# Kernel optimization log

Hardware: AMD Instinct MI355X
Metric: run time of the kernel (lower is better)

The kernel has to match this reference:

```python
import jax, jax.numpy as jnp
import numpy as np

N_NODES = 100000


def gcn_conv(x, W, b, src, dst, n):
    # PyG GCNConv: add self-loops, symmetric deg^-1/2 normalization,
    # transform then gather/scatter-add aggregate.
    loop = jnp.arange(n, dtype=src.dtype)
    s = jnp.concatenate([src, loop])
    d = jnp.concatenate([dst, loop])
    deg = jax.ops.segment_sum(jnp.ones_like(d, dtype=x.dtype), d, num_segments=n)
    dinv = jnp.where(deg > 0, 1.0 / jnp.sqrt(deg), 0.0)
    norm = dinv[s] * dinv[d]                      # [E+N]
    h = x @ W                                     # [N, out]
    msgs = h[s] * norm[:, None]                   # gather + scale
    out = jax.ops.segment_sum(msgs, d, num_segments=n)  # scatter-add
    return out + b


def setup_inputs() -> dict:
    key = jax.random.key(0)
    k1, k2, k3, k4 = jax.random.split(key, 4)
    F_in, H, D = 128, 16, 128
    x = jax.random.normal(k1, (N_NODES, F_in), dtype=jnp.float32)
    edge_index = jax.random.randint(k2, (2, 1600000), 0, N_NODES, dtype=jnp.int64)
    W1 = jax.random.normal(k3, (F_in, H), dtype=jnp.float32) / np.sqrt(F_in)
    b1 = jnp.zeros((H,), dtype=jnp.float32)
    W2 = jax.random.normal(k4, (H, D), dtype=jnp.float32) / np.sqrt(H)
    b2 = jnp.zeros((D,), dtype=jnp.float32)
    return {"x": x, "edge_index": edge_index, "W1": W1, "b1": b1, "W2": W2, "b2": b2}


def reference(x, edge_index, W1, b1, W2, b2):
    src, dst = edge_index[0], edge_index[1]
    n = x.shape[0]
    h = jax.nn.relu(gcn_conv(x, W1, b1, src, dst, n))
    out = jax.nn.relu(gcn_conv(h, W2, b2, src, dst, n))
    return out
```

## Files before the change

kernel.cpp:

```cpp
#include <hip/hip_runtime.h>
#include <hip/hip_fp16.h>
#include <stdint.h>

#define F_IN  128
#define HID   16
#define F_OUT 128
#define NBK   512
#define NBLK  512
#define BCAP  4096
#define CHUNK_MAX 4096
#define EPT   16

__device__ __forceinline__ int bucket_of(int d, int N) {
    return (int)(((long long)d * NBK) / N);
}
__device__ __forceinline__ int bucket_lo(int b, int N) {
    return (int)(((long long)b * N + NBK - 1) / NBK);
}

__global__ void __launch_bounds__(256) k_partf(
        const int* __restrict__ ei, int* __restrict__ bcur,
        uint32_t* __restrict__ pairs, int E, int N) {
    __shared__ int lh[NBK];
    __shared__ int lofs[NBK];
    __shared__ int lcur[NBK];
    __shared__ int gbase[NBK];
    __shared__ int lnlo[NBK];
    __shared__ int loff[256];
    __shared__ uint32_t spairs[CHUNK_MAX];
    __shared__ uint16_t sbkt[CHUNK_MAX];

    int blk = blockIdx.x, t = threadIdx.x;
    int C = (E + NBLK - 1) / NBLK;
    int e0 = blk * C;
    int e1 = e0 + C; if (e1 > E) e1 = E;
    int ecnt = e1 - e0;

    for (int i = t; i < NBK; i += 256) { lh[i] = 0; lnlo[i] = bucket_lo(i, N); }
    __syncthreads();

    int es[EPT], ed[EPT], eb[EPT];
#pragma unroll
    for (int k = 0; k < EPT; ++k) {
        int e = e0 + k * 256 + t;
        if (e < e1) {
            es[k] = ei[e];
            ed[k] = ei[E + e];
            eb[k] = bucket_of(ed[k], N);
            atomicAdd(&lh[eb[k]], 1);
        } else eb[k] = -1;
    }
    __syncthreads();

    int a0 = lh[2 * t], a1 = lh[2 * t + 1];
    int s2 = a0 + a1;
    loff[t] = s2;
    __syncthreads();
    for (int o = 1; o < 256; o <<= 1) {
        int a = (t >= o) ? loff[t - o] : 0;
        __syncthreads();
        loff[t] += a;
        __syncthreads();
    }
    int excl = loff[t] - s2;
    lofs[2 * t]     = excl;
    lofs[2 * t + 1] = excl + a0;
    lcur[2 * t]     = excl;
    lcur[2 * t + 1] = excl + a0;
    __syncthreads();

    for (int w = 0; w < NBK; w += 256) {
        int i = (t + w + blk) & (NBK - 1);
        int h = lh[i];
        gbase[i] = h ? atomicAdd(&bcur[i], h) : 0;
    }

#pragma unroll
    for (int k = 0; k < EPT; ++k) {
        if (eb[k] >= 0) {
            int b = eb[k];
            int idx = atomicAdd(&lcur[b], 1);
            spairs[idx] = ((uint32_t)es[k] << 10) | (uint32_t)(ed[k] - lnlo[b]);
            sbkt[idx]   = (uint16_t)b;
        }
    }
    __syncthreads();

    for (int i = t; i < ecnt; i += 256) {
        int b = sbkt[i];
        int pos = gbase[b] + (i - lofs[b]);
        if (pos < BCAP)
            pairs[(size_t)b * BCAP + pos] = spairs[i];
    }
}

__global__ void __launch_bounds__(256) k_csr2(
        const uint32_t* __restrict__ pairs, const int* __restrict__ bcur,
        int* __restrict__ row_start, int* __restrict__ cnt,
        float* __restrict__ dinv, int* __restrict__ srcs, int N) {
    __shared__ int lcnt[256];
    __shared__ int loff[256];
    __shared__ int lcur[256];
    int b = blockIdx.x, t = threadIdx.x;
    int base = b * BCAP;
    int ec = bcur[b]; if (ec > BCAP) ec = BCAP;
    int nlo = bucket_lo(b, N);
    int nhi = bucket_lo(b + 1, N); if (nhi > N) nhi = N;
    int nn = nhi - nlo;
    lcnt[t] = 0;
    __syncthreads();
    for (int e = t; e < ec; e += 256)
        atomicAdd(&lcnt[pairs[base + e] & 1023u], 1);
    __syncthreads();
    int v = lcnt[t];
    int pv = (v + 3) & ~3;
    loff[t] = pv;
    __syncthreads();
    for (int o = 1; o < 256; o <<= 1) {
        int a = (t >= o) ? loff[t - o] : 0;
        __syncthreads();
        loff[t] += a;
        __syncthreads();
    }
    if (t < nn) {
        int gs = base + (loff[t] - pv);
        row_start[nlo + t] = gs;
        cnt[nlo + t]       = v;
        dinv[nlo + t]      = rsqrtf((float)(v + 1));
        lcur[t]            = gs;
    }
    __syncthreads();
    for (int e = t; e < ec; e += 256) {
        uint32_t p = pairs[base + e];
        int pos = atomicAdd(&lcur[p & 1023u], 1);
        srcs[pos] = (int)(p >> 10);
    }
}

#define XP1 132
__global__ void __launch_bounds__(256) k_transform1(
        const float* __restrict__ x, const float* __restrict__ W1,
        const float* __restrict__ dinv, __half* __restrict__ g1, int n) {
    __shared__ float sX[32 * XP1];
    __shared__ float sWt[HID * XP1];
    int t = threadIdx.x;
    int node0 = blockIdx.x * 32;
    for (int i = t; i < F_IN * HID; i += 256) {
        int k = i >> 4, f = i & 15;
        sWt[f * XP1 + k] = W1[i];
    }
    const float4* x4 = (const float4*)(x + (size_t)node0 * F_IN);
    int nrem = n - node0;
#pragma unroll
    for (int j = 0; j < 4; ++j) {
        int idx4 = t + j * 256;
        int nl = idx4 >> 5;
        int kk = (idx4 & 31) * 4;
        float4 v = make_float4(0.f, 0.f, 0.f, 0.f);
        if (nl < nrem) v = x4[idx4];
        *(float4*)&sX[nl * XP1 + kk] = v;
    }
    __syncthreads();
    int f  = t & 7;
    int nl = t >> 3;
    float a0 = 0.f, a1 = 0.f;
    const float* xr  = &sX[nl * XP1];
    const float* wr0 = &sWt[f * XP1];
    const float* wr1 = &sWt[(f + 8) * XP1];
#pragma unroll 4
    for (int k = 0; k < F_IN; k += 4) {
        float4 xv = *(const float4*)(xr + k);
        float4 w0 = *(const float4*)(wr0 + k);
        float4 w1 = *(const float4*)(wr1 + k);
        a0 += xv.x * w0.x + xv.y * w0.y + xv.z * w0.z + xv.w * w0.w;
        a1 += xv.x * w1.x + xv.y * w1.y + xv.z * w1.z + xv.w * w1.w;
    }
    int node = node0 + nl;
    if (node < n) {
        float di = dinv[node];
        g1[(size_t)node * HID + f]     = __float2half(di * a0);
        g1[(size_t)node * HID + f + 8] = __float2half(di * a1);
    }
}

__device__ __forceinline__ void add_h8(float* __restrict__ acc, const __half* __restrict__ ptr) {
    uint4 u = *(const uint4*)ptr;
    const __half2* h = (const __half2*)&u;
#pragma unroll
    for (int q = 0; q < 4; ++q) {
        float2 f = __half22float2(h[q]);
        acc[2 * q]     += f.x;
        acc[2 * q + 1] += f.y;
    }
}

template<bool EP1>
__global__ void __launch_bounds__(256) k_gather_h(
        const __half* __restrict__ g, const int* __restrict__ srcs,
        const int* __restrict__ row_start, const int* __restrict__ cnt,
        const float* __restrict__ dinv, const float* __restrict__ b1,
        __half* __restrict__ outb, int n) {
    int t = blockIdx.x * blockDim.x + threadIdx.x;
    int node = t >> 1;
    int p = t & 1;
    if (node >= n) return;
    int rs  = row_start[node];
    int deg = cnt[node];
    float acc[8];
    {
        uint4 u = *(const uint4*)(g + (size_t)node * HID + p * 8);
        const __half2* h = (const __half2*)&u;
#pragma unroll
        for (int q = 0; q < 4; ++q) {
            float2 f = __half22float2(h[q]);
            acc[2 * q] = f.x; acc[2 * q + 1] = f.y;
        }
    }
    int j = 0;
    for (; j + 8 <= deg; j += 8) {
        int4 ia = *(const int4*)(srcs + rs + j);
        int4 ib = *(const int4*)(srcs + rs + j + 4);
        add_h8(acc, g + (size_t)ia.x * HID + p * 8);
        add_h8(acc, g + (size_t)ia.y * HID + p * 8);
        add_h8(acc, g + (size_t)ia.z * HID + p * 8);
        add_h8(acc, g + (size_t)ia.w * HID + p * 8);
        add_h8(acc, g + (size_t)ib.x * HID + p * 8);
        add_h8(acc, g + (size_t)ib.y * HID + p * 8);
        add_h8(acc, g + (size_t)ib.z * HID + p * 8);
        add_h8(acc, g + (size_t)ib.w * HID + p * 8);
    }
    if (j + 4 <= deg) {
        int4 ia = *(const int4*)(srcs + rs + j);
        add_h8(acc, g + (size_t)ia.x * HID + p * 8);
        add_h8(acc, g + (size_t)ia.y * HID + p * 8);
        add_h8(acc, g + (size_t)ia.z * HID + p * 8);
        add_h8(acc, g + (size_t)ia.w * HID + p * 8);
        j += 4;
    }
    for (; j < deg; ++j)
        add_h8(acc, g + (size_t)srcs[rs + j] * HID + p * 8);
    if (EP1) {
        float di = dinv[node];
#pragma unroll
        for (int i = 0; i < 8; ++i)
            acc[i] = di * fmaxf(di * acc[i] + b1[p * 8 + i], 0.0f);
    }
    uint4 o;
    __half2* oh = (__half2*)&o;
#pragma unroll
    for (int q = 0; q < 4; ++q)
        oh[q] = __floats2half2_rn(acc[2 * q], acc[2 * q + 1]);
    *(uint4*)(outb + (size_t)node * HID + p * 8) = o;
}

__global__ void __launch_bounds__(256) k_transform2(
        const __half* __restrict__ agg, const float* __restrict__ W2,
        const float* __restrict__ b2, const float* __restrict__ dinv,
        float* __restrict__ out, int n) {
    int t = threadIdx.x;
    int d = t & 127;
    int h = t >> 7;
    int node0 = blockIdx.x * 32;
    float wcol[HID];
#pragma unroll
    for (int f = 0; f < HID; ++f) wcol[f] = W2[f * F_OUT + d];
    float bd = b2[d];
#pragma unroll 4
    for (int i = 0; i < 16; ++i) {
        int node = node0 + h + 2 * i;
        if (node >= n) continue;
        const uint4* av = (const uint4*)(agg + (size_t)node * HID);
        uint4 u0 = av[0], u1 = av[1];
        const __half2* h0 = (const __half2*)&u0;
        const __half2* h1 = (const __half2*)&u1;
        float s = 0.f;
#pragma unroll
        for (int q = 0; q < 4; ++q) {
            float2 f0 = __half22float2(h0[q]);
            float2 f1 = __half22float2(h1[q]);
            s += f0.x * wcol[2 * q]     + f0.y * wcol[2 * q + 1];
            s += f1.x * wcol[8 + 2 * q] + f1.y * wcol[9 + 2 * q];
        }
        out[(size_t)node * F_OUT + d] = fmaxf(dinv[node] * s + bd, 0.0f);
    }
}

extern "C" void kernel_launch(void* const* d_in, const int* in_sizes, int n_in,
                              void* d_out, int out_size, void* d_ws, size_t ws_size,
                              hipStream_t stream) {
    const float* x  = (const float*)d_in[0];
    const int*   ei = (const int*)d_in[1];
    const float* W1 = (const float*)d_in[2];
    const float* b1 = (const float*)d_in[3];
    const float* W2 = (const float*)d_in[4];
    const float* b2 = (const float*)d_in[5];
    float* out = (float*)d_out;

    const int N = in_sizes[0] / F_IN;
    const int E = in_sizes[1] / 2;

    float* dinv      = (float*)d_ws;
    int*   cnt       = (int*)(dinv + N);
    int*   row_start = cnt + N;
    int*   bcur      = row_start + N;
    int*   srcs      = bcur + NBK;
    uintptr_t xb = (uintptr_t)(srcs + (size_t)NBK * BCAP + 64);
    xb = (xb + 15) & ~(uintptr_t)15;
    uint32_t* pairs = (uint32_t*)xb;
    __half* bufA = (__half*)xb;
    __half* bufB = bufA + (size_t)N * HID;

    hipMemsetAsync(bcur, 0, NBK * sizeof(int), stream);
    k_partf<<<NBLK, 256, 0, stream>>>(ei, bcur, pairs, E, N);
    k_csr2 <<<NBK, 256, 0, stream>>>(pairs, bcur, row_start, cnt, dinv, srcs, N);

    k_transform1<<<(N + 31) / 32, 256, 0, stream>>>(x, W1, dinv, bufA, N);
    k_gather_h<true> <<<((size_t)N * 2 + 255) / 256, 256, 0, stream>>>(
        bufA, srcs, row_start, cnt, dinv, b1, bufB, N);
    k_gather_h<false><<<((size_t)N * 2 + 255) / 256, 256, 0, stream>>>(
        bufB, srcs, row_start, cnt, dinv, b1, bufA, N);
    k_transform2<<<(N + 31) / 32, 256, 0, stream>>>(bufA, W2, b2, dinv, out, N);
}
```

Before: 211.0 us.

## Fuse all GCN phases into one cooperative persistent kernel with grid syncs

Replaces the memset and six separate kernel launches with a single cooperative kernel of 512 blocks. The phases (partition, CSR build, transform1, two gathers, transform2) run back to back, separated by grid.sync, and use grid-stride loops. This removes launch overhead and inter-kernel gaps. In exchange it caps parallelism at 512 blocks for the gather and transform phases, and it pays grid-barrier costs. If the cooperative launch fails, it falls back to the multi-kernel path.

```diff
diff --git a/kernel.cpp b/kernel.cpp
--- a/kernel.cpp
+++ b/kernel.cpp
@@ -1,6 +1,9 @@
 #include <hip/hip_runtime.h>
 #include <hip/hip_fp16.h>
+#include <hip/hip_cooperative_groups.h>
 #include <stdint.h>
+
+namespace cg = cooperative_groups;
 
 #define F_IN  128
 #define HID   16
@@ -10,6 +13,9 @@
 #define BCAP  4096
 #define CHUNK_MAX 4096
 #define EPT   16
+#define XP1   132
+
+static_assert(NBLK == NBK, "csr phase needs block==bucket");
 
 __device__ __forceinline__ int bucket_of(int d, int N) {
     return (int)(((long long)d * NBK) / N);
@@ -18,25 +24,28 @@
     return (int)(((long long)b * N + NBK - 1) / NBK);
 }
 
-__global__ void __launch_bounds__(256) k_partf(
-        const int* __restrict__ ei, int* __restrict__ bcur,
-        uint32_t* __restrict__ pairs, int E, int N) {
-    __shared__ int lh[NBK];
-    __shared__ int lofs[NBK];
-    __shared__ int lcur[NBK];
-    __shared__ int gbase[NBK];
-    __shared__ int lnlo[NBK];
-    __shared__ int loff[256];
-    __shared__ uint32_t spairs[CHUNK_MAX];
-    __shared__ uint16_t sbkt[CHUNK_MAX];
-
-    int blk = blockIdx.x, t = threadIdx.x;
+struct SmemPartf {
+    int lh[NBK], lofs[NBK], lcur[NBK], gbase[NBK], lnlo[NBK];
+    int loff[256];
+    uint32_t spairs[CHUNK_MAX];
+    uint16_t sbkt[CHUNK_MAX];
+};
+struct SmemCsr { int lcnt[256], loff[256], lcur[256]; };
+struct SmemT1  { float sX[32 * XP1]; float sWt[HID * XP1]; };
+
+constexpr unsigned SMEM_BYTES =
+    sizeof(SmemPartf) > sizeof(SmemT1) ? sizeof(SmemPartf) : sizeof(SmemT1);
+
+__device__ void phase_partf(char* smem, int blk, int t,
+                            const int* __restrict__ ei, int* __restrict__ bcur,
+                            uint32_t* __restrict__ pairs, int E, int N) {
+    SmemPartf* sp = (SmemPartf*)smem;
     int C = (E + NBLK - 1) / NBLK;
     int e0 = blk * C;
     int e1 = e0 + C; if (e1 > E) e1 = E;
     int ecnt = e1 - e0;
 
-    for (int i = t; i < NBK; i += 256) { lh[i] = 0; lnlo[i] = bucket_lo(i, N); }
+    for (int i = t; i < NBK; i += 256) { sp->lh[i] = 0; sp->lnlo[i] = bucket_lo(i, N); }
     __syncthreads();
 
     int es[EPT], ed[EPT], eb[EPT];
@@ -47,139 +56,137 @@
             es[k] = ei[e];
             ed[k] = ei[E + e];
             eb[k] = bucket_of(ed[k], N);
-            atomicAdd(&lh[eb[k]], 1);
+            atomicAdd(&sp->lh[eb[k]], 1);
         } else eb[k] = -1;
     }
     __syncthreads();
 
-    int a0 = lh[2 * t], a1 = lh[2 * t + 1];
+    int a0 = sp->lh[2 * t], a1 = sp->lh[2 * t + 1];
     int s2 = a0 + a1;
-    loff[t] = s2;
+    sp->loff[t] = s2;
     __syncthreads();
     for (int o = 1; o < 256; o <<= 1) {
-        int a = (t >= o) ? loff[t - o] : 0;
-        __syncthreads();
-        loff[t] += a;
-        __syncthreads();
-    }
-    int excl = loff[t] - s2;
-    lofs[2 * t]     = excl;
-    lofs[2 * t + 1] = excl + a0;
-    lcur[2 * t]     = excl;
-    lcur[2 * t + 1] = excl + a0;
+        int a = (t >= o) ? sp->loff[t - o] : 0;
+        __syncthreads();
+        sp->loff[t] += a;
+        __syncthreads();
+    }
+    int excl = sp->loff[t] - s2;
+    sp->lofs[2 * t]     = excl;
+    sp->lofs[2 * t + 1] = excl + a0;
+    sp->lcur[2 * t]     = excl;
+    sp->lcur[2 * t + 1] = excl + a0;
     __syncthreads();
 
     for (int w = 0; w < NBK; w += 256) {
         int i = (t + w + blk) & (NBK - 1);
-        int h = lh[i];
-        gbase[i] = h ? atomicAdd(&bcur[i], h) : 0;
+        int h = sp->lh[i];
+        sp->gbase[i] = h ? atomicAdd(&bcur[i], h) : 0;
     }
 
 #pragma unroll
     for (int k = 0; k < EPT; ++k) {
         if (eb[k] >= 0) {
             int b = eb[k];
-            int idx = atomicAdd(&lcur[b], 1);
-            spairs[idx] = ((uint32_t)es[k] << 10) | (uint32_t)(ed[k] - lnlo[b]);
-            sbkt[idx]   = (uint16_t)b;
+            int idx = atomicAdd(&sp->lcur[b], 1);
+            sp->spairs[idx] = ((uint32_t)es[k] << 10) | (uint32_t)(ed[k] - sp->lnlo[b]);
+            sp->sbkt[idx]   = (uint16_t)b;
         }
     }
     __syncthreads();
 
     for (int i = t; i < ecnt; i += 256) {
-        int b = sbkt[i];
-        int pos = gbase[b] + (i - lofs[b]);
+        int b = sp->sbkt[i];
+        int pos = sp->gbase[b] + (i - sp->lofs[b]);
         if (pos < BCAP)
-            pairs[(size_t)b * BCAP + pos] = spairs[i];
-    }
-}
-
-__global__ void __launch_bounds__(256) k_csr2(
-        const uint32_t* __restrict__ pairs, const int* __restrict__ bcur,
-        int* __restrict__ row_start, int* __restrict__ cnt,
-        float* __restrict__ dinv, int* __restrict__ srcs, int N) {
-    __shared__ int lcnt[256];
-    __shared__ int loff[256];
-    __shared__ int lcur[256];
-    int b = blockIdx.x, t = threadIdx.x;
+            pairs[(size_t)b * BCAP + pos] = sp->spairs[i];
+    }
+}
+
+__device__ void phase_csr(char* smem, int b, int t,
+                          const uint32_t* __restrict__ pairs, const int* __restrict__ bcur,
+                          int* __restrict__ row_start, int* __restrict__ cnt,
+                          float* __restrict__ dinv, int* __restrict__ srcs, int N) {
+    SmemCsr* sc = (SmemCsr*)smem;
     int base = b * BCAP;
     int ec = bcur[b]; if (ec > BCAP) ec = BCAP;
     int nlo = bucket_lo(b, N);
     int nhi = bucket_lo(b + 1, N); if (nhi > N) nhi = N;
     int nn = nhi - nlo;
-    lcnt[t] = 0;
+    sc->lcnt[t] = 0;
     __syncthreads();
     for (int e = t; e < ec; e += 256)
-        atomicAdd(&lcnt[pairs[base + e] & 1023u], 1);
-    __syncthreads();
-    int v = lcnt[t];
+        atomicAdd(&sc->lcnt[pairs[base + e] & 1023u], 1);
+    __syncthreads();
+    int v = sc->lcnt[t];
     int pv = (v + 3) & ~3;
-    loff[t] = pv;
+    sc->loff[t] = pv;
     __syncthreads();
     for (int o = 1; o < 256; o <<= 1) {
-        int a = (t >= o) ? loff[t - o] : 0;
-        __syncthreads();
-        loff[t] += a;
+        int a = (t >= o) ? sc->loff[t - o] : 0;
+        __syncthreads();
+        sc->loff[t] += a;
         __syncthreads();
     }
     if (t < nn) {
-        int gs = base + (loff[t] - pv);
+        int gs = base + (sc->loff[t] - pv);
         row_start[nlo + t] = gs;
         cnt[nlo + t]       = v;
         dinv[nlo + t]      = rsqrtf((float)(v + 1));
-        lcur[t]            = gs;
+        sc->lcur[t]        = gs;
     }
     __syncthreads();
     for (int e = t; e < ec; e += 256) {
         uint32_t p = pairs[base + e];
-        int pos = atomicAdd(&lcur[p & 1023u], 1);
+        int pos = atomicAdd(&sc->lcur[p & 1023u], 1);
         srcs[pos] = (int)(p >> 10);
     }
 }
 
-#define XP1 132
-__global__ void __launch_bounds__(256) k_transform1(
-        const float* __restrict__ x, const float* __restrict__ W1,
-        const float* __restrict__ dinv, __half* __restrict__ g1, int n) {
-    __shared__ float sX[32 * XP1];
-    __shared__ float sWt[HID * XP1];
-    int t = threadIdx.x;
-    int node0 = blockIdx.x * 32;
+__device__ void phase_t1(char* smem, int blk, int nblk, int t,
+                         const float* __restrict__ x, const float* __restrict__ W1,
+                         const float* __restrict__ dinv, __half* __restrict__ g1, int n) {
+    SmemT1* st = (SmemT1*)smem;
     for (int i = t; i < F_IN * HID; i += 256) {
         int k = i >> 4, f = i & 15;
-        sWt[f * XP1 + k] = W1[i];
-    }
-    const float4* x4 = (const float4*)(x + (size_t)node0 * F_IN);
-    int nrem = n - node0;
-#pragma unroll
-    for (int j = 0; j < 4; ++j) {
-        int idx4 = t + j * 256;
-        int nl = idx4 >> 5;
-        int kk = (idx4 & 31) * 4;
-        float4 v = make_float4(0.f, 0.f, 0.f, 0.f);
-        if (nl < nrem) v = x4[idx4];
-        *(float4*)&sX[nl * XP1 + kk] = v;
-    }
-    __syncthreads();
+        st->sWt[f * XP1 + k] = W1[i];
+    }
+    int nvb = (n + 31) / 32;
     int f  = t & 7;
     int nl = t >> 3;
-    float a0 = 0.f, a1 = 0.f;
-    const float* xr  = &sX[nl * XP1];
-    const float* wr0 = &sWt[f * XP1];
-    const float* wr1 = &sWt[(f + 8) * XP1];
+    for (int vb = blk; vb < nvb; vb += nblk) {
+        __syncthreads();
+        int node0 = vb * 32;
+        const float4* x4 = (const float4*)(x + (size_t)node0 * F_IN);
+        int nrem = n - node0;
+#pragma unroll
+        for (int j = 0; j < 4; ++j) {
+            int idx4 = t + j * 256;
+            int nl2 = idx4 >> 5;
+            int kk = (idx4 & 31) * 4;
+            float4 v = make_float4(0.f, 0.f, 0.f, 0.f);
+            if (nl2 < nrem) v = x4[idx4];
+            *(float4*)&st->sX[nl2 * XP1 + kk] = v;
+        }
+        __syncthreads();
+        float a0 = 0.f, a1 = 0.f;
+        const float* xr  = &st->sX[nl * XP1];
+        const float* wr0 = &st->sWt[f * XP1];
+        const float* wr1 = &st->sWt[(f + 8) * XP1];
 #pragma unroll 4
-    for (int k = 0; k < F_IN; k += 4) {
-        float4 xv = *(const float4*)(xr + k);
-        float4 w0 = *(const float4*)(wr0 + k);
-        float4 w1 = *(const float4*)(wr1 + k);
-        a0 += xv.x * w0.x + xv.y * w0.y + xv.z * w0.z + xv.w * w0.w;
-        a1 += xv.x * w1.x + xv.y * w1.y + xv.z * w1.z + xv.w * w1.w;
-    }
-    int node = node0 + nl;
-    if (node < n) {
-        float di = dinv[node];
-        g1[(size_t)node * HID + f]     = __float2half(di * a0);
-        g1[(size_t)node * HID + f + 8] = __float2half(di * a1);
+        for (int k = 0; k < F_IN; k += 4) {
+            float4 xv = *(const float4*)(xr + k);
+            float4 w0 = *(const float4*)(wr0 + k);
+            float4 w1 = *(const float4*)(wr1 + k);
+            a0 += xv.x * w0.x + xv.y * w0.y + xv.z * w0.z + xv.w * w0.w;
+            a1 += xv.x * w1.x + xv.y * w1.y + xv.z * w1.z + xv.w * w1.w;
+        }
+        int node = node0 + nl;
+        if (node < n) {
+            float di = dinv[node];
+            g1[(size_t)node * HID + f]     = __float2half(di * a0);
+            g1[(size_t)node * HID + f + 8] = __float2half(di * a1);
+        }
     }
 }
 
@@ -195,14 +202,13 @@
 }
 
 template<bool EP1>
-__global__ void __launch_bounds__(256) k_gather_h(
-        const __half* __restrict__ g, const int* __restrict__ srcs,
+__device__ __forceinline__ void gather_one(
+        int tt, const __half* __restrict__ g, const int* __restrict__ srcs,
         const int* __restrict__ row_start, const int* __restrict__ cnt,
         const float* __restrict__ dinv, const float* __restrict__ b1,
         __half* __restrict__ outb, int n) {
-    int t = blockIdx.x * blockDim.x + threadIdx.x;
-    int node = t >> 1;
-    int p = t & 1;
+    int node = tt >> 1;
+    int p = tt & 1;
     if (node >= n) return;
     int rs  = row_start[node];
     int deg = cnt[node];
@@ -253,36 +259,108 @@
     *(uint4*)(outb + (size_t)node * HID + p * 8) = o;
 }
 
-__global__ void __launch_bounds__(256) k_transform2(
-        const __half* __restrict__ agg, const float* __restrict__ W2,
-        const float* __restrict__ b2, const float* __restrict__ dinv,
-        float* __restrict__ out, int n) {
-    int t = threadIdx.x;
+__device__ void phase_t2(int blk, int nblk, int t,
+                         const __half* __restrict__ agg, const float* __restrict__ W2,
+                         const float* __restrict__ b2, const float* __restrict__ dinv,
+                         float* __restrict__ out, int n) {
     int d = t & 127;
     int h = t >> 7;
-    int node0 = blockIdx.x * 32;
     float wcol[HID];
 #pragma unroll
     for (int f = 0; f < HID; ++f) wcol[f] = W2[f * F_OUT + d];
     float bd = b2[d];
+    int nvb = (n + 31) / 32;
+    for (int vb = blk; vb < nvb; vb += nblk) {
+        int node0 = vb * 32;
 #pragma unroll 4
-    for (int i = 0; i < 16; ++i) {
-        int node = node0 + h + 2 * i;
-        if (node >= n) continue;
-        const uint4* av = (const uint4*)(agg + (size_t)node * HID);
-        uint4 u0 = av[0], u1 = av[1];
-        const __half2* h0 = (const __half2*)&u0;
-        const __half2* h1 = (const __half2*)&u1;
-        float s = 0.f;
-#pragma unroll
-        for (int q = 0; q < 4; ++q) {
-            float2 f0 = __half22float2(h0[q]);
-            float2 f1 = __half22float2(h1[q]);
-            s += f0.x * wcol[2 * q]     + f0.y * wcol[2 * q + 1];
-            s += f1.x * wcol[8 + 2 * q] + f1.y * wcol[9 + 2 * q];
-        }
-        out[(size_t)node * F_OUT + d] = fmaxf(dinv[node] * s + bd, 0.0f);
-    }
+        for (int i = 0; i < 16; ++i) {
+            int node = node0 + h + 2 * i;
+            if (node >= n) continue;
+            const uint4* av = (const uint4*)(agg + (size_t)node * HID);
+            uint4 u0 = av[0], u1 = av[1];
+            const __half2* h0 = (const __half2*)&u0;
+            const __half2* h1 = (const __half2*)&u1;
+            float s = 0.f;
+#pragma unroll
+            for (int q = 0; q < 4; ++q) {
+                float2 f0 = __half22float2(h0[q]);
+                float2 f1 = __half22float2(h1[q]);
+                s += f0.x * wcol[2 * q]     + f0.y * wcol[2 * q + 1];
+                s += f1.x * wcol[8 + 2 * q] + f1.y * wcol[9 + 2 * q];
+            }
+            out[(size_t)node * F_OUT + d] = fmaxf(dinv[node] * s + bd, 0.0f);
+        }
+    }
+}
+
+__global__ void __launch_bounds__(256) k_fused(
+        const float* __restrict__ x, const int* __restrict__ ei,
+        const float* __restrict__ W1, const float* __restrict__ b1,
+        const float* __restrict__ W2, const float* __restrict__ b2,
+        float* __restrict__ out,
+        float* dinv, int* cnt, int* row_start, int* bcur, int* srcs,
+        uint32_t* pairs, __half* bufA, __half* bufB, int N, int E) {
+    extern __shared__ char smem[];
+    cg::grid_group grid = cg::this_grid();
+    const int t = threadIdx.x, blk = blockIdx.x;
+
+    if (t == 0) bcur[blk] = 0;
+    grid.sync();
+
+    phase_partf(smem, blk, t, ei, bcur, pairs, E, N);
+    grid.sync();
+
+    phase_csr(smem, blk, t, pairs, bcur, row_start, cnt, dinv, srcs, N);
+    grid.sync();
+
+    phase_t1(smem, blk, gridDim.x, t, x, W1, dinv, bufA, N);
+    grid.sync();
+
+    {
+        int gtid = blk * 256 + t, nthr = gridDim.x * 256;
+        for (int tt = gtid; tt < 2 * N; tt += nthr)
+            gather_one<true>(tt, bufA, srcs, row_start, cnt, dinv, b1, bufB, N);
+    }
+    grid.sync();
+    {
+        int gtid = blk * 256 + t, nthr = gridDim.x * 256;
+        for (int tt = gtid; tt < 2 * N; tt += nthr)
+            gather_one<false>(tt, bufB, srcs, row_start, cnt, dinv, b1, bufA, N);
+    }
+    grid.sync();
+
+    phase_t2(blk, gridDim.x, t, bufA, W2, b2, dinv, out, N);
+}
+
+__global__ void __launch_bounds__(256) k_partf_s(const int* ei, int* bcur,
+                                                 uint32_t* pairs, int E, int N) {
+    extern __shared__ char smem[];
+    phase_partf(smem, blockIdx.x, threadIdx.x, ei, bcur, pairs, E, N);
+}
+__global__ void __launch_bounds__(256) k_csr_s(const uint32_t* pairs, const int* bcur,
+                                               int* row_start, int* cnt, float* dinv,
+                                               int* srcs, int N) {
+    extern __shared__ char smem[];
+    phase_csr(smem, blockIdx.x, threadIdx.x, pairs, bcur, row_start, cnt, dinv, srcs, N);
+}
+__global__ void __launch_bounds__(256) k_t1_s(const float* x, const float* W1,
+                                              const float* dinv, __half* g1, int n) {
+    extern __shared__ char smem[];
+    phase_t1(smem, blockIdx.x, gridDim.x, threadIdx.x, x, W1, dinv, g1, n);
+}
+template<bool EP1>
+__global__ void __launch_bounds__(256) k_gather_s(const __half* g, const int* srcs,
+                                                  const int* row_start, const int* cnt,
+                                                  const float* dinv, const float* b1,
+                                                  __half* outb, int n) {
+    int tt = blockIdx.x * 256 + threadIdx.x;
+    if (tt < 2 * n)
+        gather_one<EP1>(tt, g, srcs, row_start, cnt, dinv, b1, outb, n);
+}
+__global__ void __launch_bounds__(256) k_t2_s(const __half* agg, const float* W2,
+                                              const float* b2, const float* dinv,
+                                              float* out, int n) {
+    phase_t2(blockIdx.x, gridDim.x, threadIdx.x, agg, W2, b2, dinv, out, n);
 }
 
 extern "C" void kernel_launch(void* const* d_in, const int* in_sizes, int n_in,
@@ -296,8 +374,8 @@
     const float* b2 = (const float*)d_in[5];
     float* out = (float*)d_out;
 
-    const int N = in_sizes[0] / F_IN;
-    const int E = in_sizes[1] / 2;
+    int N = in_sizes[0] / F_IN;
+    int E = in_sizes[1] / 2;
 
     float* dinv      = (float*)d_ws;
     int*   cnt       = (int*)(dinv + N);
@@ -310,14 +388,24 @@
     __half* bufA = (__half*)xb;
     __half* bufB = bufA + (size_t)N * HID;
 
-    hipMemsetAsync(bcur, 0, NBK * sizeof(int), stream);
-    k_partf<<<NBLK, 256, 0, stream>>>(ei, bcur, pairs, E, N);
-    k_csr2 <<<NBK, 256, 0, stream>>>(pairs, bcur, row_start, cnt, dinv, srcs, N);
-
-    k_transform1<<<(N + 31) / 32, 256, 0, stream>>>(x, W1, dinv, bufA, N);
-    k_gather_h<true> <<<((size_t)N * 2 + 255) / 256, 256, 0, stream>>>(
-        bufA, srcs, row_start, cnt, dinv, b1, bufB, N);
-    k_gather_h<false><<<((size_t)N * 2 + 255) / 256, 256, 0, stream>>>(
-        bufB, srcs, row_start, cnt, dinv, b1, bufA, N);
-    k_transform2<<<(N + 31) / 32, 256, 0, stream>>>(bufA, W2, b2, dinv, out, N);
-}
+    void* kargs[] = {
+        (void*)&x, (void*)&ei, (void*)&W1, (void*)&b1, (void*)&W2, (void*)&b2,
+        (void*)&out, (void*)&dinv, (void*)&cnt, (void*)&row_start, (void*)&bcur,
+        (void*)&srcs, (void*)&pairs, (void*)&bufA, (void*)&bufB,
+        (void*)&N, (void*)&E
+    };
+    hipError_t err = hipLaunchCooperativeKernel((const void*)k_fused,
+                                                dim3(NBLK), dim3(256),
+                                                kargs, SMEM_BYTES, stream);
+    if (err != hipSuccess) {
+        hipMemsetAsync(bcur, 0, NBK * sizeof(int), stream);
+        k_partf_s<<<NBLK, 256, sizeof(SmemPartf), stream>>>(ei, bcur, pairs, E, N);
+        k_csr_s <<<NBK, 256, sizeof(SmemCsr), stream>>>(pairs, bcur, row_start, cnt, dinv, srcs, N);
+        k_t1_s  <<<(N + 31) / 32, 256, sizeof(SmemT1), stream>>>(x, W1, dinv, bufA, N);
+        k_gather_s<true> <<<((size_t)N * 2 + 255) / 256, 256, 0, stream>>>(
+            bufA, srcs, row_start, cnt, dinv, b1, bufB, N);
+        k_gather_s<false><<<((size_t)N * 2 + 255) / 256, 256, 0, stream>>>(
+            bufB, srcs, row_start, cnt, dinv, b1, bufA, N);
+        k_t2_s  <<<(N + 31) / 32, 256, 0, stream>>>(bufA, W2, b2, dinv, out, N);
+    }
+}
```

Result: slower. 617.6 us (+192.6%).

## Fuse CSR build with first transform and second gather with output transform

Applied to the files above, without the earlier changes.

Merges the per-bucket CSR construction with the first dense transform, so each bucket block computes g1 for its own node range using dinv already held in shared memory. Fuses the second aggregation with the final 16x128 transform, keeping aggregated rows in shared memory and writing float4 outputs. Two kernel launches and an intermediate half buffer round trip are removed. In exchange the first transform now runs on only 512 blocks, which lowers parallelism, and buffers no longer alias the pairs region, so the workspace grows.

```diff
diff --git a/kernel.cpp b/kernel.cpp
--- a/kernel.cpp
+++ b/kernel.cpp
@@ -10,6 +10,8 @@
 #define BCAP  4096
 #define CHUNK_MAX 4096
 #define EPT   16
+#define XP1   132
+#define GT2_NODES 128
 
 __device__ __forceinline__ int bucket_of(int d, int N) {
     return (int)(((long long)d * NBK) / N);
@@ -21,11 +23,7 @@
 __global__ void __launch_bounds__(256) k_partf(
         const int* __restrict__ ei, int* __restrict__ bcur,
         uint32_t* __restrict__ pairs, int E, int N) {
-    __shared__ int lh[NBK];
-    __shared__ int lofs[NBK];
-    __shared__ int lcur[NBK];
-    __shared__ int gbase[NBK];
-    __shared__ int lnlo[NBK];
+    __shared__ int lh[NBK], lofs[NBK], lcur[NBK], gbase[NBK], lnlo[NBK];
     __shared__ int loff[256];
     __shared__ uint32_t spairs[CHUNK_MAX];
     __shared__ uint16_t sbkt[CHUNK_MAX];
@@ -94,92 +92,96 @@
     }
 }
 
-__global__ void __launch_bounds__(256) k_csr2(
+__global__ void __launch_bounds__(256) k_csr_t1(
         const uint32_t* __restrict__ pairs, const int* __restrict__ bcur,
+        const float* __restrict__ x, const float* __restrict__ W1,
         int* __restrict__ row_start, int* __restrict__ cnt,
-        float* __restrict__ dinv, int* __restrict__ srcs, int N) {
-    __shared__ int lcnt[256];
-    __shared__ int loff[256];
-    __shared__ int lcur[256];
+        float* __restrict__ dinv, int* __restrict__ srcs,
+        __half* __restrict__ g1, int N) {
+    __shared__ union {
+        struct { int lcnt[256]; int loff[256]; int lcur[256]; } c;
+        struct { float sX[32 * XP1]; float sWt[HID * XP1]; } t1;
+    } u;
+    __shared__ float sdinv[224];
+
     int b = blockIdx.x, t = threadIdx.x;
     int base = b * BCAP;
     int ec = bcur[b]; if (ec > BCAP) ec = BCAP;
     int nlo = bucket_lo(b, N);
     int nhi = bucket_lo(b + 1, N); if (nhi > N) nhi = N;
     int nn = nhi - nlo;
-    lcnt[t] = 0;
+
+    u.c.lcnt[t] = 0;
     __syncthreads();
     for (int e = t; e < ec; e += 256)
-        atomicAdd(&lcnt[pairs[base + e] & 1023u], 1);
-    __syncthreads();
-    int v = lcnt[t];
+        atomicAdd(&u.c.lcnt[pairs[base + e] & 1023u], 1);
+    __syncthreads();
+    int v = u.c.lcnt[t];
     int pv = (v + 3) & ~3;
-    loff[t] = pv;
+    u.c.loff[t] = pv;
     __syncthreads();
     for (int o = 1; o < 256; o <<= 1) {
-        int a = (t >= o) ? loff[t - o] : 0;
-        __syncthreads();
-        loff[t] += a;
+        int a = (t >= o) ? u.c.loff[t - o] : 0;
+        __syncthreads();
+        u.c.loff[t] += a;
         __syncthreads();
     }
     if (t < nn) {
-        int gs = base + (loff[t] - pv);
+        int gs = base + (u.c.loff[t] - pv);
         row_start[nlo + t] = gs;
         cnt[nlo + t]       = v;
-        dinv[nlo + t]      = rsqrtf((float)(v + 1));
-        lcur[t]            = gs;
+        float dv = rsqrtf((float)(v + 1));
+        dinv[nlo + t]      = dv;
+        sdinv[t]           = dv;
+        u.c.lcur[t]        = gs;
     }
     __syncthreads();
     for (int e = t; e < ec; e += 256) {
         uint32_t p = pairs[base + e];
-        int pos = atomicAdd(&lcur[p & 1023u], 1);
+        int pos = atomicAdd(&u.c.lcur[p & 1023u], 1);
         srcs[pos] = (int)(p >> 10);
     }
-}
-
-#define XP1 132
-__global__ void __launch_bounds__(256) k_transform1(
-        const float* __restrict__ x, const float* __restrict__ W1,
-        const float* __restrict__ dinv, __half* __restrict__ g1, int n) {
-    __shared__ float sX[32 * XP1];
-    __shared__ float sWt[HID * XP1];
-    int t = threadIdx.x;
-    int node0 = blockIdx.x * 32;
+    __syncthreads();
+
     for (int i = t; i < F_IN * HID; i += 256) {
         int k = i >> 4, f = i & 15;
-        sWt[f * XP1 + k] = W1[i];
-    }
-    const float4* x4 = (const float4*)(x + (size_t)node0 * F_IN);
-    int nrem = n - node0;
-#pragma unroll
-    for (int j = 0; j < 4; ++j) {
-        int idx4 = t + j * 256;
-        int nl = idx4 >> 5;
-        int kk = (idx4 & 31) * 4;
-        float4 v = make_float4(0.f, 0.f, 0.f, 0.f);
-        if (nl < nrem) v = x4[idx4];
-        *(float4*)&sX[nl * XP1 + kk] = v;
-    }
-    __syncthreads();
+        u.t1.sWt[f * XP1 + k] = W1[i];
+    }
     int f  = t & 7;
     int nl = t >> 3;
-    float a0 = 0.f, a1 = 0.f;
-    const float* xr  = &sX[nl * XP1];
-    const float* wr0 = &sWt[f * XP1];
-    const float* wr1 = &sWt[(f + 8) * XP1];
+    for (int c0 = 0; c0 < nn; c0 += 32) {
+        __syncthreads();
+        int node0 = nlo + c0;
+        int nrem = nn - c0;
+        const float4* x4 = (const float4*)(x + (size_t)node0 * F_IN);
+#pragma unroll
+        for (int j = 0; j < 4; ++j) {
+            int idx4 = t + j * 256;
+            int nl2 = idx4 >> 5;
+            int kk = (idx4 & 31) * 4;
+            float4 vv = make_float4(0.f, 0.f, 0.f, 0.f);
+            if (nl2 < nrem) vv = x4[idx4];
+            *(float4*)&u.t1.sX[nl2 * XP1 + kk] = vv;
+        }
+        __syncthreads();
+        float a0 = 0.f, a1 = 0.f;
+        const float* xr  = &u.t1.sX[nl * XP1];
+        const float* wr0 = &u.t1.sWt[f * XP1];
+        const float* wr1 = &u.t1.sWt[(f + 8) * XP1];
 #pragma unroll 4
-    for (int k = 0; k < F_IN; k += 4) {
-        float4 xv = *(const float4*)(xr + k);
-        float4 w0 = *(const float4*)(wr0 + k);
-        float4 w1 = *(const float4*)(wr1 + k);
-        a0 += xv.x * w0.x + xv.y * w0.y + xv.z * w0.z + xv.w * w0.w;
-        a1 += xv.x * w1.x + xv.y * w1.y + xv.z * w1.z + xv.w * w1.w;
-    }
-    int node = node0 + nl;
-    if (node < n) {
-        float di = dinv[node];
-        g1[(size_t)node * HID + f]     = __float2half(di * a0);
-        g1[(size_t)node * HID + f + 8] = __float2half(di * a1);
+        for (int k = 0; k < F_IN; k += 4) {
+            float4 xv = *(const float4*)(xr + k);
+            float4 w0 = *(const float4*)(wr0 + k);
+            float4 w1 = *(const float4*)(wr1 + k);
+            a0 += xv.x * w0.x + xv.y * w0.y + xv.z * w0.z + xv.w * w0.w;
+            a1 += xv.x * w1.x + xv.y * w1.y + xv.z * w1.z + xv.w * w1.w;
+        }
+        if (nl < nrem) {
+            int node = node0 + nl;
+            float di = sdinv[c0 + nl];
+            g1[(size_t)node * HID + f]     = __float2half(di * a0);
+            g1[(size_t)node * HID + f + 8] = __float2half(di * a1);
+        }
     }
 }
 
@@ -194,19 +196,10 @@
     }
 }
 
-template<bool EP1>
-__global__ void __launch_bounds__(256) k_gather_h(
+__device__ __forceinline__ void gather_acc(
+        float* __restrict__ acc, int node, int p,
         const __half* __restrict__ g, const int* __restrict__ srcs,
-        const int* __restrict__ row_start, const int* __restrict__ cnt,
-        const float* __restrict__ dinv, const float* __restrict__ b1,
-        __half* __restrict__ outb, int n) {
-    int t = blockIdx.x * blockDim.x + threadIdx.x;
-    int node = t >> 1;
-    int p = t & 1;
-    if (node >= n) return;
-    int rs  = row_start[node];
-    int deg = cnt[node];
-    float acc[8];
+        int rs, int deg) {
     {
         uint4 u = *(const uint4*)(g + (size_t)node * HID + p * 8);
         const __half2* h = (const __half2*)&u;
@@ -239,12 +232,23 @@
     }
     for (; j < deg; ++j)
         add_h8(acc, g + (size_t)srcs[rs + j] * HID + p * 8);
-    if (EP1) {
-        float di = dinv[node];
-#pragma unroll
-        for (int i = 0; i < 8; ++i)
-            acc[i] = di * fmaxf(di * acc[i] + b1[p * 8 + i], 0.0f);
-    }
+}
+
+__global__ void __launch_bounds__(256) k_gather1(
+        const __half* __restrict__ g, const int* __restrict__ srcs,
+        const int* __restrict__ row_start, const int* __restrict__ cnt,
+        const float* __restrict__ dinv, const float* __restrict__ b1,
+        __half* __restrict__ outb, int n) {
+    int tt = blockIdx.x * 256 + threadIdx.x;
+    int node = tt >> 1;
+    int p = tt & 1;
+    if (node >= n) return;
+    float acc[8];
+    gather_acc(acc, node, p, g, srcs, row_start[node], cnt[node]);
+    float di = dinv[node];
+#pragma unroll
+    for (int i = 0; i < 8; ++i)
+        acc[i] = di * fmaxf(di * acc[i] + b1[p * 8 + i], 0.0f);
     uint4 o;
     __half2* oh = (__half2*)&o;
 #pragma unroll
@@ -253,35 +257,63 @@
     *(uint4*)(outb + (size_t)node * HID + p * 8) = o;
 }
 
-__global__ void __launch_bounds__(256) k_transform2(
-        const __half* __restrict__ agg, const float* __restrict__ W2,
-        const float* __restrict__ b2, const float* __restrict__ dinv,
-        float* __restrict__ out, int n) {
+__global__ void __launch_bounds__(256) k_gather_t2(
+        const __half* __restrict__ g, const int* __restrict__ srcs,
+        const int* __restrict__ row_start, const int* __restrict__ cnt,
+        const float* __restrict__ dinv, const float* __restrict__ W2,
+        const float* __restrict__ b2, float* __restrict__ out, int n) {
+    __shared__ __half sAgg[GT2_NODES * HID];
+    __shared__ float  sdv[GT2_NODES];
     int t = threadIdx.x;
-    int d = t & 127;
-    int h = t >> 7;
-    int node0 = blockIdx.x * 32;
-    float wcol[HID];
-#pragma unroll
-    for (int f = 0; f < HID; ++f) wcol[f] = W2[f * F_OUT + d];
-    float bd = b2[d];
+    int node0 = blockIdx.x * GT2_NODES;
+
+    {
+        int nl = t >> 1, p = t & 1;
+        int node = node0 + nl;
+        if (node < n) {
+            if (p == 0) sdv[nl] = dinv[node];
+            float acc[8];
+            gather_acc(acc, node, p, g, srcs, row_start[node], cnt[node]);
+            uint4 o;
+            __half2* oh = (__half2*)&o;
+#pragma unroll
+            for (int q = 0; q < 4; ++q)
+                oh[q] = __floats2half2_rn(acc[2 * q], acc[2 * q + 1]);
+            *(uint4*)&sAgg[nl * HID + p * 8] = o;
+        }
+    }
+    __syncthreads();
+
+    int d0 = (t & 31) * 4;
+    int h  = t >> 5;
+    float4 wcv[HID];
+#pragma unroll
+    for (int f2 = 0; f2 < HID; ++f2)
+        wcv[f2] = *(const float4*)(W2 + f2 * F_OUT + d0);
+    float4 bv = *(const float4*)(b2 + d0);
 #pragma unroll 4
-    for (int i = 0; i < 16; ++i) {
-        int node = node0 + h + 2 * i;
+    for (int i = 0; i < GT2_NODES / 8; ++i) {
+        int nl = h + 8 * i;
+        int node = node0 + nl;
         if (node >= n) continue;
-        const uint4* av = (const uint4*)(agg + (size_t)node * HID);
-        uint4 u0 = av[0], u1 = av[1];
-        const __half2* h0 = (const __half2*)&u0;
-        const __half2* h1 = (const __half2*)&u1;
-        float s = 0.f;
-#pragma unroll
-        for (int q = 0; q < 4; ++q) {
-            float2 f0 = __half22float2(h0[q]);
-            float2 f1 = __half22float2(h1[q]);
-            s += f0.x * wcol[2 * q]     + f0.y * wcol[2 * q + 1];
-            s += f1.x * wcol[8 + 2 * q] + f1.y * wcol[9 + 2 * q];
-        }
-        out[(size_t)node * F_OUT + d] = fmaxf(dinv[node] * s + bd, 0.0f);
+        const __half2* ah = (const __half2*)&sAgg[nl * HID];
+        float4 s = make_float4(0.f, 0.f, 0.f, 0.f);
+#pragma unroll
+        for (int f2 = 0; f2 < HID; f2 += 2) {
+            float2 fa = __half22float2(ah[f2 >> 1]);
+            float4 w0 = wcv[f2], w1 = wcv[f2 + 1];
+            s.x += fa.x * w0.x + fa.y * w1.x;
+            s.y += fa.x * w0.y + fa.y * w1.y;
+            s.z += fa.x * w0.z + fa.y * w1.z;
+            s.w += fa.x * w0.w + fa.y * w1.w;
+        }
+        float dv = sdv[nl];
+        float4 ov;
+        ov.x = fmaxf(dv * s.x + bv.x, 0.f);
+        ov.y = fmaxf(dv * s.y + bv.y, 0.f);
+        ov.z = fmaxf(dv * s.z + bv.z, 0.f);
+        ov.w = fmaxf(dv * s.w + bv.w, 0.f);
+        *(float4*)(out + (size_t)node * F_OUT + d0) = ov;
     }
 }
 
@@ -304,20 +336,16 @@
     int*   row_start = cnt + N;
     int*   bcur      = row_start + N;
     int*   srcs      = bcur + NBK;
-    uintptr_t xb = (uintptr_t)(srcs + (size_t)NBK * BCAP + 64);
-    xb = (xb + 15) & ~(uintptr_t)15;
-    uint32_t* pairs = (uint32_t*)xb;
-    __half* bufA = (__half*)xb;
-    __half* bufB = bufA + (size_t)N * HID;
+    uint32_t* pairs  = (uint32_t*)(srcs + (size_t)NBK * BCAP);
+    __half* bufA     = (__half*)(pairs + (size_t)NBK * BCAP);
+    __half* bufB     = bufA + (size_t)N * HID;
 
     hipMemsetAsync(bcur, 0, NBK * sizeof(int), stream);
     k_partf<<<NBLK, 256, 0, stream>>>(ei, bcur, pairs, E, N);
-    k_csr2 <<<NBK, 256, 0, stream>>>(pairs, bcur, row_start, cnt, dinv, srcs, N);
-
-    k_transform1<<<(N + 31) / 32, 256, 0, stream>>>(x, W1, dinv, bufA, N);
-    k_gather_h<true> <<<((size_t)N * 2 + 255) / 256, 256, 0, stream>>>(
+    k_csr_t1<<<NBK, 256, 0, stream>>>(pairs, bcur, x, W1,
+                                      row_start, cnt, dinv, srcs, bufA, N);
+    k_gather1<<<((size_t)N * 2 + 255) / 256, 256, 0, stream>>>(
         bufA, srcs, row_start, cnt, dinv, b1, bufB, N);
-    k_gather_h<false><<<((size_t)N * 2 + 255) / 256, 256, 0, stream>>>(
-        bufB, srcs, row_start, cnt, dinv, b1, bufA, N);
-    k_transform2<<<(N + 31) / 32, 256, 0, stream>>>(bufA, W2, b2, dinv, out, N);
-}
+    k_gather_t2<<<(N + GT2_NODES - 1) / GT2_NODES, 256, 0, stream>>>(
+        bufB, srcs, row_start, cnt, dinv, W2, b2, out, N);
+}
```

Measured after the change: 210.9 us. About the same (-0.1%).
